# Kernel tuning notes

Measured on AMD Instinct MI355X. Metric: run time of the kernel, lower is better.

The kernel has to match this reference:

```python
import jax, jax.numpy as jnp
import numpy as np

EMB = 1024

def setup_inputs() -> dict:
    key = jax.random.key(0)
    ks = jax.random.split(key, 6)
    B, S, E = 4, 2048, EMB
    x = jax.random.normal(ks[0], (B, S, E), dtype=jnp.float32)
    attention_mask = jax.random.randint(ks[1], (B, S, S), 0, 2, dtype=jnp.int32)
    proj_w = jax.random.normal(ks[2], (E, 3 * E), dtype=jnp.float32) * (1.0 / np.sqrt(E))
    proj_b = jax.random.normal(ks[3], (3 * E,), dtype=jnp.float32) * 0.02
    out_w = jax.random.normal(ks[4], (E, E), dtype=jnp.float32) * (1.0 / np.sqrt(E))
    out_b = jax.random.normal(ks[5], (E,), dtype=jnp.float32) * 0.02
    return {"x": x, "attention_mask": attention_mask, "proj_w": proj_w,
            "proj_b": proj_b, "out_w": out_w, "out_b": out_b}

def reference(x, attention_mask, proj_w, proj_b, out_w, out_b):
    E = x.shape[-1]
    scale = 1.0 / jnp.sqrt(jnp.asarray(E, x.dtype))
    qkv = x @ proj_w + proj_b                      # [B,S,3E]
    q, k, v = jnp.split(qkv, 3, axis=-1)           # each [B,S,E]
    scores = jnp.einsum('bqe,bke->bqk', q, k) * scale  # [B,S,S]
    scores = jnp.where(attention_mask == 0, jnp.asarray(-1e20, scores.dtype), scores)
    attn = jax.nn.softmax(scores, axis=-1)
    ctx = jnp.einsum('bqk,bke->bqe', attn, v)      # [B,S,E]
    return ctx @ out_w + out_b
```

## Files before the change

kernel.cpp:

```cpp
#include <hip/hip_runtime.h>
#include <cstdint>

typedef unsigned short u16;
typedef uint32_t u32;
typedef __bf16 bf16x8 __attribute__((ext_vector_type(8)));
typedef float f32x4 __attribute__((ext_vector_type(4)));

__device__ __forceinline__ u16 f2bf(float f) {
  unsigned u = __float_as_uint(f);
  u += 0x7fffu + ((u >> 16) & 1u);
  return (u16)(u >> 16);
}

__device__ __forceinline__ void async16(const void* g, void* l) {
  __builtin_amdgcn_global_load_lds(
      (const __attribute__((address_space(1))) uint32_t*)g,
      (__attribute__((address_space(3))) uint32_t*)l, 16, 0, 0);
}

__global__ void k_cvt(const float* __restrict__ in, u16* __restrict__ out, int n4) {
  int i = blockIdx.x * blockDim.x + threadIdx.x;
  if (i >= n4) return;
  const float4 v = ((const float4*)in)[i];
  ushort4 o;
  o.x = f2bf(v.x); o.y = f2bf(v.y); o.z = f2bf(v.z); o.w = f2bf(v.w);
  ((ushort4*)out)[i] = o;
}

__device__ __forceinline__ u16 to_bf(float v) { return f2bf(v); }
__device__ __forceinline__ u16 to_bf(u16 v) { return v; }

template <typename Tin>
__global__ void k_transpose(const Tin* __restrict__ in, u16* __restrict__ out,
                            int lda, int ldo, long bsIn, long bsOut) {
  __shared__ u16 tile[32][33];
  const int b = blockIdx.z;
  in += (size_t)b * bsIn;
  out += (size_t)b * bsOut;
  const int c0 = blockIdx.x * 32, r0 = blockIdx.y * 32;
  const int tx = threadIdx.x, ty = threadIdx.y;
#pragma unroll
  for (int i = 0; i < 4; ++i) {
    int r = r0 + ty + i * 8;
    tile[ty + i * 8][tx] = to_bf(in[(size_t)r * lda + c0 + tx]);
  }
  __syncthreads();
#pragma unroll
  for (int i = 0; i < 4; ++i) {
    out[(size_t)(c0 + ty + i * 8) * ldo + r0 + tx] = tile[tx][ty + i * 8];
  }
}

__global__ __launch_bounds__(256) void k_bitpack(const int* __restrict__ mask,
                                                 u32* __restrict__ mbits) {
  const size_t w = (size_t)blockIdx.x * 256 + threadIdx.x;
  const int* p = mask + w * 32;
  u32 bits = 0;
#pragma unroll
  for (int j = 0; j < 8; ++j) {
    const int4 v = ((const int4*)p)[j];
    bits |= (u32)(v.x & 1) << (j * 4 + 0);
    bits |= (u32)(v.y & 1) << (j * 4 + 1);
    bits |= (u32)(v.z & 1) << (j * 4 + 2);
    bits |= (u32)(v.w & 1) << (j * 4 + 3);
  }
  mbits[w] = bits;
}

template <int MODE>
__global__ __launch_bounds__(256) void gemm_bt(
    const u16* __restrict__ A, long lda, long bsA,
    const u16* __restrict__ Bt, long ldb, long bsB,
    void* __restrict__ C, long ldc, long bsC,
    int M, int N, int K,
    const float* __restrict__ bias, const u32* __restrict__ mbits) {
  __shared__ u16 As[128 * 64];
  __shared__ u16 Bs[128 * 64];

  const int b = blockIdx.z;
  const int m0 = blockIdx.y * 128, n0 = blockIdx.x * 128;
  const int lane = threadIdx.x & 63;
  const int w = threadIdx.x >> 6;
  const int wr = w >> 1, wc = w & 1;

  const int srow = lane >> 3;
  const int scol = ((lane & 7) ^ ((lane >> 3) & 7)) * 8;
  const u16* pa = A + (size_t)b * bsA + (size_t)(m0 + srow) * lda + scol;
  const u16* pb = Bt + (size_t)b * bsB + (size_t)(n0 + srow) * ldb + scol;

  const int m_l = lane & 15, q = lane >> 4, m7 = m_l & 7;
  const int offs[2] = {(q ^ m7) * 8, ((4 + q) ^ m7) * 8};

  f32x4 acc[4][4] = {};
  f32x4 accs[4] = {};
  bf16x8 ones;
#pragma unroll
  for (int e = 0; e < 8; ++e) ones[e] = (__bf16)1.0f;

  for (int kt = 0; kt < K; kt += 64) {
    __syncthreads();
#pragma unroll
    for (int g = 0; g < 4; ++g) {
      const int c = w * 4 + g;
      async16(pa + (size_t)(c * 8) * lda, As + c * 512);
      async16(pb + (size_t)(c * 8) * ldb, Bs + c * 512);
    }
    __syncthreads();
#pragma unroll
    for (int s = 0; s < 2; ++s) {
      bf16x8 af[4], bfr[4];
#pragma unroll
      for (int t = 0; t < 4; ++t)
        af[t] = *(const bf16x8*)(As + (wr * 64 + t * 16 + m_l) * 64 + offs[s]);
#pragma unroll
      for (int t = 0; t < 4; ++t)
        bfr[t] = *(const bf16x8*)(Bs + (wc * 64 + t * 16 + m_l) * 64 + offs[s]);
#pragma unroll
      for (int mt = 0; mt < 4; ++mt)
#pragma unroll
        for (int nt = 0; nt < 4; ++nt)
          acc[mt][nt] = __builtin_amdgcn_mfma_f32_16x16x32_bf16(af[mt], bfr[nt], acc[mt][nt], 0, 0, 0);
      if constexpr (MODE == 2) {
#pragma unroll
        for (int mt = 0; mt < 4; ++mt)
          accs[mt] = __builtin_amdgcn_mfma_f32_16x16x32_bf16(af[mt], ones, accs[mt], 0, 0, 0);
      }
    }
    pa += 64;
    pb += 64;
  }

  if constexpr (MODE == 1) {
    __syncthreads();
    const int rl = threadIdx.x >> 1, pr = threadIdx.x & 1;
    const uint2 v = *(const uint2*)(mbits + ((size_t)(b * M + m0 + rl)) * (N >> 5) + (n0 >> 5) + pr * 2);
    ((u32*)As)[rl * 4 + pr * 2] = v.x;
    ((u32*)As)[rl * 4 + pr * 2 + 1] = v.y;
    __syncthreads();
  }

  float rinv[4][4];
  if constexpr (MODE == 2) {
#pragma unroll
    for (int mt = 0; mt < 4; ++mt)
#pragma unroll
      for (int r = 0; r < 4; ++r) rinv[mt][r] = 1.0f / accs[mt][r];
  }

#pragma unroll
  for (int mt = 0; mt < 4; ++mt) {
#pragma unroll
    for (int nt = 0; nt < 4; ++nt) {
      const int col = n0 + wc * 64 + nt * 16 + m_l;
      const int row0 = m0 + wr * 64 + mt * 16 + q * 4;
#pragma unroll
      for (int r = 0; r < 4; ++r) {
        const int row = row0 + r;
        float v = acc[mt][nt][r];
        if constexpr (MODE == 0) {
          v += bias[col];
          if (col < 1024) v *= 0.03125f;
          ((u16*)C)[(size_t)b * bsC + (size_t)row * ldc + col] = f2bf(v);
        } else if constexpr (MODE == 1) {
          const int cl = wc * 64 + nt * 16 + m_l;
          const int rl = wr * 64 + mt * 16 + q * 4 + r;
          const u32 wb = ((const u32*)As)[rl * 4 + (cl >> 5)];
          v = ((wb >> (cl & 31)) & 1u) ? __expf(fminf(v, 30.f)) : 0.f;
          ((u16*)C)[(size_t)b * bsC + (size_t)row * ldc + col] = f2bf(v);
        } else if constexpr (MODE == 2) {
          v *= rinv[mt][r];
          ((u16*)C)[(size_t)b * bsC + (size_t)row * ldc + col] = f2bf(v);
        } else {
          v += bias[col];
          ((float*)C)[(size_t)b * bsC + (size_t)row * ldc + col] = v;
        }
      }
    }
  }
}

extern "C" void kernel_launch(void* const* d_in, const int* in_sizes, int n_in,
                              void* d_out, int out_size, void* d_ws, size_t ws_size,
                              hipStream_t stream) {
  const float* x = (const float*)d_in[0];
  const int* mask = (const int*)d_in[1];
  const float* proj_w = (const float*)d_in[2];
  const float* proj_b = (const float*)d_in[3];
  const float* out_w = (const float*)d_in[4];
  const float* out_b = (const float*)d_in[5];
  float* out = (float*)d_out;

  char* ws = (char*)d_ws;
  u16* xb = (u16*)(ws);
  u16* wt = (u16*)(ws + 16777216);
  u16* owt = (u16*)(ws + 23068672);
  u16* qkv = (u16*)(ws + 25165824);
  u16* P = (u16*)(ws + 75497472);
  u16* Vt = (u16*)(ws + 109051904);
  u16* ctx = xb;
  u32* mbits = (u32*)wt;

  k_cvt<<<8192, 256, 0, stream>>>(x, xb, 2097152);
  k_transpose<float><<<dim3(96, 32, 1), dim3(32, 8), 0, stream>>>(proj_w, wt, 3072, 1024, 0, 0);
  k_transpose<float><<<dim3(32, 32, 1), dim3(32, 8), 0, stream>>>(out_w, owt, 1024, 1024, 0, 0);
  gemm_bt<0><<<dim3(24, 64, 1), 256, 0, stream>>>(xb, 1024, 0, wt, 1024, 0, qkv, 3072, 0,
                                                  8192, 3072, 1024, proj_b, nullptr);
  k_bitpack<<<2048, 256, 0, stream>>>(mask, mbits);
  k_transpose<u16><<<dim3(32, 64, 4), dim3(32, 8), 0, stream>>>(
      qkv + 2048, Vt, 3072, 2048, (long)2048 * 3072, (long)1024 * 2048);
  gemm_bt<1><<<dim3(16, 16, 4), 256, 0, stream>>>(
      qkv, 3072, (long)2048 * 3072, qkv + 1024, 3072, (long)2048 * 3072,
      P, 2048, (long)2048 * 2048, 2048, 2048, 1024, nullptr, mbits);
  gemm_bt<2><<<dim3(8, 16, 4), 256, 0, stream>>>(
      P, 2048, (long)2048 * 2048, Vt, 2048, (long)1024 * 2048,
      ctx, 1024, (long)2048 * 1024, 2048, 1024, 2048, nullptr, nullptr);
  gemm_bt<3><<<dim3(8, 64, 1), 256, 0, stream>>>(ctx, 1024, 0, owt, 1024, 0, out, 1024, 0,
                                                 8192, 1024, 1024, out_b, nullptr);
}
```

Baseline: 349.4 us.

## Reassociate output projection into V and fuse prep conversions into one kernel

The output projection is reassociated as P·(V·Wo): a new GEMM computes U = V·Wo and writes it transposed in bf16, which removes both the separate V transpose and the final ctx·Wo GEMM. The softmax-normalising PV GEMM now adds the output bias and writes fp32 straight to the output. The x conversion and both weight transposes are merged into a single launch. This cuts launches and intermediate traffic, at the cost of an extra rounding of V·Wo to bf16 before the attention-weighted sum.

```diff
diff --git a/kernel.cpp b/kernel.cpp
--- a/kernel.cpp
+++ b/kernel.cpp
@@ -18,37 +18,39 @@
       (__attribute__((address_space(3))) uint32_t*)l, 16, 0, 0);
 }
 
-__global__ void k_cvt(const float* __restrict__ in, u16* __restrict__ out, int n4) {
-  int i = blockIdx.x * blockDim.x + threadIdx.x;
-  if (i >= n4) return;
-  const float4 v = ((const float4*)in)[i];
-  ushort4 o;
-  o.x = f2bf(v.x); o.y = f2bf(v.y); o.z = f2bf(v.z); o.w = f2bf(v.w);
-  ((ushort4*)out)[i] = o;
-}
-
-__device__ __forceinline__ u16 to_bf(float v) { return f2bf(v); }
-__device__ __forceinline__ u16 to_bf(u16 v) { return v; }
-
-template <typename Tin>
-__global__ void k_transpose(const Tin* __restrict__ in, u16* __restrict__ out,
-                            int lda, int ldo, long bsIn, long bsOut) {
+__global__ __launch_bounds__(256) void k_prep(const float* __restrict__ x, u16* __restrict__ xb,
+                                              const float* __restrict__ pw, u16* __restrict__ wt,
+                                              const float* __restrict__ ow, u16* __restrict__ owt) {
+  const int bid = blockIdx.x;
+  if (bid < 8192) {
+    const int i = bid * 256 + threadIdx.x;
+    const float4 v = ((const float4*)x)[i];
+    ushort4 o;
+    o.x = f2bf(v.x); o.y = f2bf(v.y); o.z = f2bf(v.z); o.w = f2bf(v.w);
+    ((ushort4*)xb)[i] = o;
+    return;
+  }
   __shared__ u16 tile[32][33];
-  const int b = blockIdx.z;
-  in += (size_t)b * bsIn;
-  out += (size_t)b * bsOut;
-  const int c0 = blockIdx.x * 32, r0 = blockIdx.y * 32;
-  const int tx = threadIdx.x, ty = threadIdx.y;
-#pragma unroll
-  for (int i = 0; i < 4; ++i) {
-    int r = r0 + ty + i * 8;
-    tile[ty + i * 8][tx] = to_bf(in[(size_t)r * lda + c0 + tx]);
-  }
+  const int tx = threadIdx.x & 31, ty = threadIdx.x >> 5;
+  const float* in;
+  u16* outp;
+  int lda, ldo, c0, r0;
+  if (bid < 11264) {
+    const int id = bid - 8192;
+    c0 = (id % 96) * 32; r0 = (id / 96) * 32;
+    in = pw; outp = wt; lda = 3072; ldo = 1024;
+  } else {
+    const int id = bid - 11264;
+    c0 = (id % 32) * 32; r0 = (id / 32) * 32;
+    in = ow; outp = owt; lda = 1024; ldo = 1024;
+  }
+#pragma unroll
+  for (int i = 0; i < 4; ++i)
+    tile[ty + i * 8][tx] = f2bf(in[(size_t)(r0 + ty + i * 8) * lda + c0 + tx]);
   __syncthreads();
 #pragma unroll
-  for (int i = 0; i < 4; ++i) {
-    out[(size_t)(c0 + ty + i * 8) * ldo + r0 + tx] = tile[tx][ty + i * 8];
-  }
+  for (int i = 0; i < 4; ++i)
+    outp[(size_t)(c0 + ty + i * 8) * ldo + r0 + tx] = tile[tx][ty + i * 8];
 }
 
 __global__ __launch_bounds__(256) void k_bitpack(const int* __restrict__ mask,
@@ -153,26 +155,30 @@
     for (int nt = 0; nt < 4; ++nt) {
       const int col = n0 + wc * 64 + nt * 16 + m_l;
       const int row0 = m0 + wr * 64 + mt * 16 + q * 4;
-#pragma unroll
-      for (int r = 0; r < 4; ++r) {
-        const int row = row0 + r;
-        float v = acc[mt][nt][r];
-        if constexpr (MODE == 0) {
-          v += bias[col];
-          if (col < 1024) v *= 0.03125f;
-          ((u16*)C)[(size_t)b * bsC + (size_t)row * ldc + col] = f2bf(v);
-        } else if constexpr (MODE == 1) {
-          const int cl = wc * 64 + nt * 16 + m_l;
-          const int rl = wr * 64 + mt * 16 + q * 4 + r;
-          const u32 wb = ((const u32*)As)[rl * 4 + (cl >> 5)];
-          v = ((wb >> (cl & 31)) & 1u) ? __expf(fminf(v, 30.f)) : 0.f;
-          ((u16*)C)[(size_t)b * bsC + (size_t)row * ldc + col] = f2bf(v);
-        } else if constexpr (MODE == 2) {
-          v *= rinv[mt][r];
-          ((u16*)C)[(size_t)b * bsC + (size_t)row * ldc + col] = f2bf(v);
-        } else {
-          v += bias[col];
-          ((float*)C)[(size_t)b * bsC + (size_t)row * ldc + col] = v;
+      if constexpr (MODE == 3) {
+        ushort4 o;
+        o.x = f2bf(acc[mt][nt][0]); o.y = f2bf(acc[mt][nt][1]);
+        o.z = f2bf(acc[mt][nt][2]); o.w = f2bf(acc[mt][nt][3]);
+        *(ushort4*)((u16*)C + (size_t)b * bsC + (size_t)col * ldc + row0) = o;
+      } else {
+#pragma unroll
+        for (int r = 0; r < 4; ++r) {
+          const int row = row0 + r;
+          float v = acc[mt][nt][r];
+          if constexpr (MODE == 0) {
+            v += bias[col];
+            if (col < 1024) v *= 0.03125f;
+            ((u16*)C)[(size_t)b * bsC + (size_t)row * ldc + col] = f2bf(v);
+          } else if constexpr (MODE == 1) {
+            const int cl = wc * 64 + nt * 16 + m_l;
+            const int rl = wr * 64 + mt * 16 + q * 4 + r;
+            const u32 wb = ((const u32*)As)[rl * 4 + (cl >> 5)];
+            v = ((wb >> (cl & 31)) & 1u) ? __expf(fminf(v, 30.f)) : 0.f;
+            ((u16*)C)[(size_t)b * bsC + (size_t)row * ldc + col] = f2bf(v);
+          } else if constexpr (MODE == 2) {
+            v = v * rinv[mt][r] + bias[col];
+            ((float*)C)[(size_t)b * bsC + (size_t)row * ldc + col] = v;
+          }
         }
       }
     }
@@ -196,24 +202,20 @@
   u16* owt = (u16*)(ws + 23068672);
   u16* qkv = (u16*)(ws + 25165824);
   u16* P = (u16*)(ws + 75497472);
-  u16* Vt = (u16*)(ws + 109051904);
-  u16* ctx = xb;
+  u16* Ut = (u16*)xb;
   u32* mbits = (u32*)wt;
 
-  k_cvt<<<8192, 256, 0, stream>>>(x, xb, 2097152);
-  k_transpose<float><<<dim3(96, 32, 1), dim3(32, 8), 0, stream>>>(proj_w, wt, 3072, 1024, 0, 0);
-  k_transpose<float><<<dim3(32, 32, 1), dim3(32, 8), 0, stream>>>(out_w, owt, 1024, 1024, 0, 0);
+  k_prep<<<12288, 256, 0, stream>>>(x, xb, proj_w, wt, out_w, owt);
   gemm_bt<0><<<dim3(24, 64, 1), 256, 0, stream>>>(xb, 1024, 0, wt, 1024, 0, qkv, 3072, 0,
                                                   8192, 3072, 1024, proj_b, nullptr);
   k_bitpack<<<2048, 256, 0, stream>>>(mask, mbits);
-  k_transpose<u16><<<dim3(32, 64, 4), dim3(32, 8), 0, stream>>>(
-      qkv + 2048, Vt, 3072, 2048, (long)2048 * 3072, (long)1024 * 2048);
   gemm_bt<1><<<dim3(16, 16, 4), 256, 0, stream>>>(
       qkv, 3072, (long)2048 * 3072, qkv + 1024, 3072, (long)2048 * 3072,
       P, 2048, (long)2048 * 2048, 2048, 2048, 1024, nullptr, mbits);
+  gemm_bt<3><<<dim3(8, 16, 4), 256, 0, stream>>>(
+      qkv + 2048, 3072, (long)2048 * 3072, owt, 1024, 0,
+      Ut, 2048, (long)1024 * 2048, 2048, 1024, 1024, nullptr, nullptr);
   gemm_bt<2><<<dim3(8, 16, 4), 256, 0, stream>>>(
-      P, 2048, (long)2048 * 2048, Vt, 2048, (long)1024 * 2048,
-      ctx, 1024, (long)2048 * 1024, 2048, 1024, 2048, nullptr, nullptr);
-  gemm_bt<3><<<dim3(8, 64, 1), 256, 0, stream>>>(ctx, 1024, 0, owt, 1024, 0, out, 1024, 0,
-                                                 8192, 1024, 1024, out_b, nullptr);
-}
+      P, 2048, (long)2048 * 2048, Ut, 2048, (long)1024 * 2048,
+      out, 1024, (long)2048 * 1024, 2048, 1024, 2048, out_b, nullptr);
+}
```

New measurement: 345.4 us. About the same (-1.2%).
